# Kernel optimization log

Measured on AMD Instinct MI355X. Metric: run time of the kernel, lower is better.

## Reference

```python
import jax, jax.numpy as jnp
import numpy as np

B, S, D = 2, 1024, 2048
MLP_RATIO = 4
N_LAYERS = 2
H = D * MLP_RATIO
EPS = 1e-5


def _act_quant(x):
    # BitNet b1.58: per-token int8 absmax quantization over last dim
    scale = 127.0 / jnp.clip(jnp.max(jnp.abs(x), axis=-1, keepdims=True), EPS, None)
    return jnp.clip(jnp.round(x * scale), -128.0, 127.0) / scale


def _weight_quant(w):
    # BitNet b1.58: per-tensor ternary quantization with mean-abs scale
    scale = 1.0 / jnp.clip(jnp.mean(jnp.abs(w)), EPS, None)
    return jnp.clip(jnp.round(w * scale), -1.0, 1.0) / scale


def _ste(v, quant_fn):
    # straight-through estimator: forward quantized, backward identity
    return v + jax.lax.stop_gradient(quant_fn(v) - v)


def bit_linear(x, w, b):
    # x: [B,S,in], w: [out,in], b: [out]
    xq = _ste(x, _act_quant)
    wq = _ste(w, _weight_quant)
    return jnp.einsum('bsi,oi->bso', xq, wq) + b


def setup_inputs() -> dict:
    key = jax.random.key(0)
    ks = jax.random.split(key, 16)
    inp = {
        'x': jax.random.normal(ks[0], (B, S, D), jnp.float32),
        'y': jax.random.normal(ks[1], (B, S, D), jnp.float32),
        'z': jax.random.normal(ks[2], (B, S, D), jnp.float32),
        'focus_mask': jax.random.uniform(ks[3], (B, S, 1), jnp.float32),
        'w_in': jax.random.normal(ks[4], (D, 3 * D), jnp.float32) * 0.02,
        'b_in': jnp.zeros((D,), jnp.float32),
        'fc1_w': jax.random.normal(ks[5], (N_LAYERS, H, D), jnp.float32) * 0.02,
        'fc1_b': jnp.zeros((N_LAYERS, H), jnp.float32),
        'fc2_w': jax.random.normal(ks[6], (N_LAYERS, D, H), jnp.float32) * 0.02,
        'fc2_b': jnp.zeros((N_LAYERS, D), jnp.float32),
        'w_out': jax.random.normal(ks[7], (D, D), jnp.float32) * 0.02,
        'b_out': jnp.zeros((D,), jnp.float32),
    }
    return inp


def reference(x, y, z, focus_mask, w_in, b_in, fc1_w, fc1_b, fc2_w, fc2_b, w_out, b_out):
    h = bit_linear(jnp.concatenate([x, y, z], axis=-1), w_in, b_in)
    for l in range(N_LAYERS):
        u = jax.nn.gelu(bit_linear(h, fc1_w[l], fc1_b[l]), approximate=False)
        h = h + bit_linear(u, fc2_w[l], fc2_b[l])
    delta = bit_linear(h, w_out, b_out)
    return y + focus_mask * delta
```

## Files before the change

### kernel.cpp

```cpp
#include <hip/hip_runtime.h>

#define EPSQ 1e-5f

typedef int i32x4 __attribute__((ext_vector_type(4)));
typedef float f32x4n __attribute__((ext_vector_type(4)));

__device__ __forceinline__ unsigned short f2bf(float f) {
  unsigned int b = __builtin_bit_cast(unsigned int, f);
  b += 0x7FFFu + ((b >> 16) & 1u);
  return (unsigned short)(b >> 16);
}
__device__ __forceinline__ float bf2f(unsigned short u) {
  unsigned int b = ((unsigned int)u) << 16;
  return __builtin_bit_cast(float, b);
}
__device__ __forceinline__ int packw4(float a, float b, float c, float d, float inv) {
  int qa = (int)fminf(fmaxf(rintf(a * inv), -1.0f), 1.0f);
  int qb = (int)fminf(fmaxf(rintf(b * inv), -1.0f), 1.0f);
  int qc = (int)fminf(fmaxf(rintf(c * inv), -1.0f), 1.0f);
  int qd = (int)fminf(fmaxf(rintf(d * inv), -1.0f), 1.0f);
  return (qa & 255) | ((qb & 255) << 8) | ((qc & 255) << 16) | ((qd & 255) << 24);
}
__device__ __forceinline__ int packa4(float a, float b, float c, float d, float s) {
  int qa = (int)fminf(fmaxf(rintf(a * s), -128.0f), 127.0f);
  int qb = (int)fminf(fmaxf(rintf(b * s), -128.0f), 127.0f);
  int qc = (int)fminf(fmaxf(rintf(c * s), -128.0f), 127.0f);
  int qd = (int)fminf(fmaxf(rintf(d * s), -128.0f), 127.0f);
  return (qa & 255) | ((qb & 255) << 8) | ((qc & 255) << 16) | ((qd & 255) << 24);
}

struct WTbl {
  const float* p[6];
  unsigned char* q[6];
  unsigned int cum[7];
};

__global__ __launch_bounds__(256) void wmean_partial(WTbl tbl, double* __restrict__ part) {
  const int b = blockIdx.x;
  int t = 0;
#pragma unroll
  for (int i = 1; i < 6; ++i) t += (b >= (int)tbl.cum[i]);
  const f32x4n* __restrict__ p = (const f32x4n*)tbl.p[t];
  const unsigned int base = (unsigned)(b - (int)tbl.cum[t]) * 2048u + threadIdx.x;
  f32x4n v[8];
#pragma unroll
  for (int u = 0; u < 8; ++u) v[u] = __builtin_nontemporal_load(p + base + (unsigned)u * 256u);
  double s = 0.0;
#pragma unroll
  for (int u = 0; u < 8; ++u)
    s += (double)(fabsf(v[u][0]) + fabsf(v[u][1])) + (double)(fabsf(v[u][2]) + fabsf(v[u][3]));
  for (int off = 32; off; off >>= 1) s += __shfl_xor(s, off);
  __shared__ double wsum[4];
  if ((threadIdx.x & 63) == 0) wsum[threadIdx.x >> 6] = s;
  __syncthreads();
  if (threadIdx.x == 0) part[b] = (wsum[0] + wsum[1]) + (wsum[2] + wsum[3]);
}

__global__ __launch_bounds__(256) void wmean_final(const double* __restrict__ part,
                                                   WTbl tbl, float* wmean) {
  for (int t = 0; t < 6; ++t) {
    const int lo = (int)tbl.cum[t], hi = (int)tbl.cum[t + 1];
    double s = 0.0;
    for (int i = lo + (int)threadIdx.x; i < hi; i += 256) s += part[i];
    for (int off = 32; off; off >>= 1) s += __shfl_xor(s, off);
    __shared__ double w4[4];
    if ((threadIdx.x & 63) == 0) w4[threadIdx.x >> 6] = s;
    __syncthreads();
    if (threadIdx.x == 0) {
      const double n = (double)(hi - lo) * 8192.0;
      float m = (float)(((w4[0] + w4[1]) + (w4[2] + w4[3])) / n);
      if (m < EPSQ) m = EPSQ;
      wmean[t] = m;
    }
    __syncthreads();
  }
}

__global__ __launch_bounds__(256) void wquant(WTbl tbl, const float* wmean) {
  const int b = blockIdx.x;
  int t = 0;
#pragma unroll
  for (int i = 1; i < 6; ++i) t += (b >= (int)tbl.cum[i]);
  const float inv = 1.0f / wmean[t];
  const f32x4n* __restrict__ p = (const f32x4n*)tbl.p[t];
  int* __restrict__ q = (int*)tbl.q[t];
  const unsigned int base = (unsigned)(b - (int)tbl.cum[t]) * 2048u + threadIdx.x;
  f32x4n v[8];
#pragma unroll
  for (int u = 0; u < 8; ++u) v[u] = __builtin_nontemporal_load(p + base + (unsigned)u * 256u);
#pragma unroll
  for (int u = 0; u < 8; ++u)
    q[base + (unsigned)u * 256u] = packw4(v[u][0], v[u][1], v[u][2], v[u][3], inv);
}

__device__ __forceinline__ float block_max256(float m) {
  for (int off = 32; off; off >>= 1) m = fmaxf(m, __shfl_xor(m, off));
  __shared__ float wm[4];
  if ((threadIdx.x & 63) == 0) wm[threadIdx.x >> 6] = m;
  __syncthreads();
  return fmaxf(fmaxf(wm[0], wm[1]), fmaxf(wm[2], wm[3]));
}

__global__ __launch_bounds__(256) void aq_cat(const float* x, const float* y, const float* z,
                                              unsigned char* q, float* rsx) {
  const int row = blockIdx.x, tid = threadIdx.x;
  const float4* px = (const float4*)(x + (size_t)row * 2048);
  const float4* py = (const float4*)(y + (size_t)row * 2048);
  const float4* pz = (const float4*)(z + (size_t)row * 2048);
  float4 v[6];
  v[0] = px[tid]; v[1] = px[tid + 256];
  v[2] = py[tid]; v[3] = py[tid + 256];
  v[4] = pz[tid]; v[5] = pz[tid + 256];
  float m = 0.0f;
#pragma unroll
  for (int k = 0; k < 6; ++k)
    m = fmaxf(m, fmaxf(fmaxf(fabsf(v[k].x), fabsf(v[k].y)), fmaxf(fabsf(v[k].z), fabsf(v[k].w))));
  m = fmaxf(block_max256(m), EPSQ);
  const float s = 127.0f / m;
  if (tid == 0) rsx[row] = m / 127.0f;
  int* qr = (int*)(q + (size_t)row * 6144);
#pragma unroll
  for (int k = 0; k < 6; ++k) qr[k * 256 + tid] = packa4(v[k].x, v[k].y, v[k].z, v[k].w, s);
}

__global__ __launch_bounds__(256) void aq_bf16(const unsigned short* u, unsigned char* q, float* rsx) {
  const int row = blockIdx.x, tid = threadIdx.x;
  const uint4* pu = (const uint4*)(u + (size_t)row * 8192);
  float f[32];
#pragma unroll
  for (int k = 0; k < 4; ++k) {
    uint4 w = pu[tid + 256 * k];
    unsigned int ws4[4] = {w.x, w.y, w.z, w.w};
#pragma unroll
    for (int j = 0; j < 4; ++j) {
      f[k * 8 + j * 2 + 0] = bf2f((unsigned short)(ws4[j] & 0xFFFFu));
      f[k * 8 + j * 2 + 1] = bf2f((unsigned short)(ws4[j] >> 16));
    }
  }
  float m = 0.0f;
#pragma unroll
  for (int k = 0; k < 32; ++k) m = fmaxf(m, fabsf(f[k]));
  m = fmaxf(block_max256(m), EPSQ);
  const float s = 127.0f / m;
  if (tid == 0) rsx[row] = m / 127.0f;
  int* qp = (int*)(q + (size_t)row * 8192);
#pragma unroll
  for (int k = 0; k < 4; ++k) {
    qp[(tid + 256 * k) * 2 + 0] = packa4(f[k * 8 + 0], f[k * 8 + 1], f[k * 8 + 2], f[k * 8 + 3], s);
    qp[(tid + 256 * k) * 2 + 1] = packa4(f[k * 8 + 4], f[k * 8 + 5], f[k * 8 + 6], f[k * 8 + 7], s);
  }
}

template<int EPI>
__global__ __launch_bounds__(256) void gemm_bt(
    const unsigned char* __restrict__ A, const unsigned char* __restrict__ Bw,
    const float* rsx, const float* wmean, const float* bias,
    float* outF, unsigned short* outB, int* outI,
    int M, int N, int K, int Ksz) {
  __shared__ unsigned char As[2][128 * 128];
  __shared__ unsigned char Bs[2][128 * 128];
  const int tid = threadIdx.x;

  const int gx = gridDim.x, gy = gridDim.y;
  const int orig = blockIdx.y * gx + blockIdx.x;
  const int xcd = orig & 7;
  const int local = orig >> 3;
  const int cn = (gx >= 32) ? 8 : 4;
  const int npx = gx / cn;
  const int n = (xcd % cn) * npx + (local % npx);
  const int m = (xcd / cn) * (gy / (8 / cn)) + (local / npx);
  const int brow = m << 7;
  const int bcol = n << 7;

  const int lane = tid & 63;
  const int wv = tid >> 6;
  const int wr = (wv >> 1) << 6;
  const int wc = (wv & 1) << 6;
  const int lr = lane & 15;
  const int lg = lane >> 4;

  i32x4 acc[4][4] = {};

  const int scol = (((tid & 7) ^ ((tid >> 3) & 7)) << 4);
  const size_t koff = (size_t)blockIdx.z * Ksz;
  const unsigned char* gA0 = A + (size_t)(brow + (tid >> 3)) * K + koff + scol;
  const unsigned char* gB0 = Bw + (size_t)(bcol + (tid >> 3)) * K + koff + scol;
  const int ldst = (tid & ~63) * 16;

  auto stage = [&](int b, int kt) {
#pragma unroll
    for (int c = 0; c < 4; ++c) {
      __builtin_amdgcn_global_load_lds(
          (const __attribute__((address_space(1))) void*)(gA0 + (size_t)kt * 128 + (size_t)c * 32 * K),
          (__attribute__((address_space(3))) void*)(&As[b][c * 4096 + ldst]),
          16, 0, 0);
      __builtin_amdgcn_global_load_lds(
          (const __attribute__((address_space(1))) void*)(gB0 + (size_t)kt * 128 + (size_t)c * 32 * K),
          (__attribute__((address_space(3))) void*)(&Bs[b][c * 4096 + ldst]),
          16, 0, 0);
    }
  };

  const int nkt = Ksz >> 7;
  stage(0, 0);
  stage(1, 1);

  for (int kt = 0; kt < nkt; ++kt) {
    const int cur = kt & 1;
    if (kt + 1 < nkt) {
      asm volatile("s_waitcnt vmcnt(8)" ::: "memory");
    } else {
      asm volatile("s_waitcnt vmcnt(0)" ::: "memory");
    }
    __builtin_amdgcn_s_barrier();
    __builtin_amdgcn_sched_barrier(0);
    __builtin_amdgcn_s_setprio(1);
#pragma unroll
    for (int kk = 0; kk < 2; ++kk) {
      i32x4 af[4], bfr[4];
#pragma unroll
      for (int i = 0; i < 4; ++i) {
        const int ra = wr + i * 16 + lr;
        const int rb = wc + i * 16 + lr;
        const int ch = (((kk << 2) | lg) ^ (lr & 7)) << 4;
        af[i]  = *(const i32x4*)(&As[cur][ra * 128 + ch]);
        bfr[i] = *(const i32x4*)(&Bs[cur][rb * 128 + ch]);
      }
#pragma unroll
      for (int i = 0; i < 4; ++i)
#pragma unroll
        for (int j = 0; j < 4; ++j)
          acc[i][j] = __builtin_amdgcn_mfma_i32_16x16x64_i8(af[i], bfr[j], acc[i][j], 0, 0, 0);
    }
    __builtin_amdgcn_s_setprio(0);
    __builtin_amdgcn_sched_barrier(0);
    __builtin_amdgcn_s_barrier();
    __builtin_amdgcn_sched_barrier(0);
    if (kt + 2 < nkt) stage(cur, kt + 2);
  }

  const float mscale = (EPI == 4) ? 0.0f : wmean[0];
  int* pI = (EPI == 4) ? (outI + (size_t)blockIdx.z * M * N) : nullptr;
#pragma unroll
  for (int i = 0; i < 4; ++i) {
#pragma unroll
    for (int r = 0; r < 4; ++r) {
      const int row = brow + wr + i * 16 + lg * 4 + r;
      const float sc = (EPI == 4) ? 1.0f : rsx[row] * mscale;
#pragma unroll
      for (int j = 0; j < 4; ++j) {
        const int col = bcol + wc + j * 16 + lr;
        const size_t o = (size_t)row * N + col;
        if constexpr (EPI == 4) {
          pI[o] = acc[i][j][r];
        } else {
          float v = (float)acc[i][j][r] * sc + bias[col];
          float g = 0.5f * v * (1.0f + erff(v * 0.70710678118654752f));
          outB[o] = f2bf(g);
        }
      }
    }
  }
}

__global__ __launch_bounds__(512, 2) void gemm_fc1(
    const unsigned char* __restrict__ A,
    const unsigned char* __restrict__ Bw,
    const float* rsx, const float* wmean, const float* bias,
    unsigned short* outB, int M, int N, int K) {
  __shared__ unsigned char As[2][256 * 128];
  __shared__ unsigned char Bs[2][256 * 128];
  const int tid = threadIdx.x;

  const int gx = gridDim.x, gy = gridDim.y;
  const int orig = blockIdx.y * gx + blockIdx.x;
  const int xcd = orig & 7;
  const int local = orig >> 3;
  const int cn = (gx >= 32) ? 8 : 4;
  const int npx = gx / cn;
  const int n = (xcd % cn) * npx + (local % npx);
  const int m = (xcd / cn) * (gy / (8 / cn)) + (local / npx);
  const int brow = m << 8;
  const int bcol = n << 8;

  const int lane = tid & 63;
  const int wv = tid >> 6;
  const int wr = (wv >> 2) << 7;
  const int wc = (wv & 3) << 6;
  const int lr = lane & 15;
  const int lg = lane >> 4;

  i32x4 acc[8][4] = {};

  const int scol = (((tid & 7) ^ ((tid >> 3) & 7)) << 4);
  const unsigned char* gA0 = A + (size_t)(brow + (tid >> 3)) * K + scol;
  const unsigned char* gB0 = Bw + (size_t)(bcol + (tid >> 3)) * K + scol;
  const int ldst = (tid & ~63) * 16;

  auto stage = [&](int b, int kt) {
#pragma unroll
    for (int c = 0; c < 4; ++c) {
      __builtin_amdgcn_global_load_lds(
          (const __attribute__((address_space(1))) void*)(gA0 + (size_t)kt * 128 + (size_t)c * 64 * K),
          (__attribute__((address_space(3))) void*)(&As[b][c * 8192 + ldst]),
          16, 0, 0);
      __builtin_amdgcn_global_load_lds(
          (const __attribute__((address_space(1))) void*)(gB0 + (size_t)kt * 128 + (size_t)c * 64 * K),
          (__attribute__((address_space(3))) void*)(&Bs[b][c * 8192 + ldst]),
          16, 0, 0);
    }
  };

  const int nkt = K >> 7;
  stage(0, 0);
  stage(1, 1);

  for (int kt = 0; kt < nkt; ++kt) {
    const int cur = kt & 1;
    if (kt + 1 < nkt) {
      asm volatile("s_waitcnt vmcnt(8)" ::: "memory");
    } else {
      asm volatile("s_waitcnt vmcnt(0)" ::: "memory");
    }
    __builtin_amdgcn_s_barrier();
    __builtin_amdgcn_sched_barrier(0);
    __builtin_amdgcn_s_setprio(1);
#pragma unroll
    for (int kk = 0; kk < 2; ++kk) {
      const int ch = (((kk << 2) | lg) ^ (lr & 7)) << 4;
      i32x4 af[8], bfr[4];
#pragma unroll
      for (int i = 0; i < 8; ++i)
        af[i] = *(const i32x4*)(&As[cur][(wr + i * 16 + lr) * 128 + ch]);
#pragma unroll
      for (int j = 0; j < 4; ++j)
        bfr[j] = *(const i32x4*)(&Bs[cur][(wc + j * 16 + lr) * 128 + ch]);
#pragma unroll
      for (int i = 0; i < 8; ++i)
#pragma unroll
        for (int j = 0; j < 4; ++j)
          acc[i][j] = __builtin_amdgcn_mfma_i32_16x16x64_i8(af[i], bfr[j], acc[i][j], 0, 0, 0);
    }
    __builtin_amdgcn_s_setprio(0);
    __builtin_amdgcn_sched_barrier(0);
    __builtin_amdgcn_s_barrier();
    __builtin_amdgcn_sched_barrier(0);
    if (kt + 2 < nkt) stage(cur, kt + 2);
  }

  const float mscale = wmean[0];
#pragma unroll
  for (int i = 0; i < 8; ++i) {
#pragma unroll
    for (int r = 0; r < 4; ++r) {
      const int row = brow + wr + i * 16 + lg * 4 + r;
      const float sc = rsx[row] * mscale;
#pragma unroll
      for (int j = 0; j < 4; ++j) {
        const int col = bcol + wc + j * 16 + lr;
        float v = (float)acc[i][j][r] * sc + bias[col];
        float g = 0.5f * v * (1.0f + erff(v * 0.70710678118654752f));
        outB[(size_t)row * N + col] = f2bf(g);
      }
    }
  }
}

template<int EPI, bool WRITE_H>
__global__ __launch_bounds__(256) void reduce_qa(
    const int* __restrict__ part, int S, size_t MN,
    const float* __restrict__ wmean, const float* __restrict__ bias,
    float* __restrict__ hbuf, float* __restrict__ rsx,
    unsigned char* __restrict__ qa) {
  const int row = blockIdx.x, tid = threadIdx.x;
  const float sc = rsx[row] * wmean[0];
  const size_t rbase = (size_t)row * 2048;
  int4 v0 = *(const int4*)(part + rbase + (size_t)tid * 4);
  int4 v1 = *(const int4*)(part + rbase + (size_t)(tid + 256) * 4);
  for (int s = 1; s < S; ++s) {
    const int* ps = part + (size_t)s * MN + rbase;
    int4 a0 = *(const int4*)(ps + (size_t)tid * 4);
    int4 a1 = *(const int4*)(ps + (size_t)(tid + 256) * 4);
    v0.x += a0.x; v0.y += a0.y; v0.z += a0.z; v0.w += a0.w;
    v1.x += a1.x; v1.y += a1.y; v1.z += a1.z; v1.w += a1.w;
  }
  const float4 b0 = *(const float4*)(bias + tid * 4);
  const float4 b1 = *(const float4*)(bias + (tid + 256) * 4);
  float4 r0, r1;
  r0.x = (float)v0.x * sc + b0.x; r0.y = (float)v0.y * sc + b0.y;
  r0.z = (float)v0.z * sc + b0.z; r0.w = (float)v0.w * sc + b0.w;
  r1.x = (float)v1.x * sc + b1.x; r1.y = (float)v1.y * sc + b1.y;
  r1.z = (float)v1.z * sc + b1.z; r1.w = (float)v1.w * sc + b1.w;
  if constexpr (EPI == 2) {
    const float4 h0 = *(const float4*)(hbuf + rbase + (size_t)tid * 4);
    const float4 h1 = *(const float4*)(hbuf + rbase + (size_t)(tid + 256) * 4);
    r0.x += h0.x; r0.y += h0.y; r0.z += h0.z; r0.w += h0.w;
    r1.x += h1.x; r1.y += h1.y; r1.z += h1.z; r1.w += h1.w;
  }
  float m = fmaxf(fmaxf(fmaxf(fabsf(r0.x), fabsf(r0.y)), fmaxf(fabsf(r0.z), fabsf(r0.w))),
                  fmaxf(fmaxf(fabsf(r1.x), fabsf(r1.y)), fmaxf(fabsf(r1.z), fabsf(r1.w))));
  m = fmaxf(block_max256(m), EPSQ);
  const float s127 = 127.0f / m;
  if (tid == 0) rsx[row] = m / 127.0f;
  if constexpr (WRITE_H) {
    *(float4*)(hbuf + rbase + (size_t)tid * 4) = r0;
    *(float4*)(hbuf + rbase + (size_t)(tid + 256) * 4) = r1;
  }
  int* qp = (int*)(qa + rbase);
  qp[tid]       = packa4(r0.x, r0.y, r0.z, r0.w, s127);
  qp[tid + 256] = packa4(r1.x, r1.y, r1.z, r1.w, s127);
}

__global__ __launch_bounds__(256) void reduce_final(
    const int* __restrict__ part, int S, int N, size_t MN,
    const float* rsx, const float* wmean, const float* bias,
    const float* aux, const float* focus, float* outF) {
  const size_t i4 = ((size_t)blockIdx.x * 256 + threadIdx.x) * 4;
  if (i4 >= MN) return;
  const int row = (int)(i4 / (unsigned)N);
  const int col = (int)(i4 % (unsigned)N);
  int4 v = *(const int4*)(part + i4);
  for (int s = 1; s < S; ++s) {
    int4 p = *(const int4*)(part + (size_t)s * MN + i4);
    v.x += p.x; v.y += p.y; v.z += p.z; v.w += p.w;
  }
  const float sc = rsx[row] * wmean[0];
  const float4 b = *(const float4*)(bias + col);
  const float4 a = *(const float4*)(aux + i4);
  const float fm = focus[row];
  float4 r;
  r.x = a.x + fm * ((float)v.x * sc + b.x);
  r.y = a.y + fm * ((float)v.y * sc + b.y);
  r.z = a.z + fm * ((float)v.z * sc + b.z);
  r.w = a.w + fm * ((float)v.w * sc + b.w);
  *(float4*)(outF + i4) = r;
}

extern "C" void kernel_launch(void* const* d_in, const int* in_sizes, int n_in,
                              void* d_out, int out_size, void* d_ws, size_t ws_size,
                              hipStream_t stream) {
  const float* x     = (const float*)d_in[0];
  const float* y     = (const float*)d_in[1];
  const float* z     = (const float*)d_in[2];
  const float* fmsk  = (const float*)d_in[3];
  const float* w_in  = (const float*)d_in[4];
  const float* b_in  = (const float*)d_in[5];
  const float* fc1_w = (const float*)d_in[6];
  const float* fc1_b = (const float*)d_in[7];
  const float* fc2_w = (const float*)d_in[8];
  const float* fc2_b = (const float*)d_in[9];
  const float* w_out = (const float*)d_in[10];
  const float* b_out = (const float*)d_in[11];
  float* out = (float*)d_out;

  const int M = 2048;
  const int D = 2048, H = 8192, K3 = 6144;
  const size_t MN = (size_t)M * D;

  char* ws = (char*)d_ws;
  size_t off = 0;
  auto alloc = [&](size_t bytes) { size_t r = off; off = (off + bytes + 255) & ~(size_t)255; return r; };
  unsigned char* wq_in   = (unsigned char*)(ws + alloc((size_t)D * K3));
  unsigned char* wq_fc10 = (unsigned char*)(ws + alloc((size_t)H * D));
  unsigned char* wq_fc11 = (unsigned char*)(ws + alloc((size_t)H * D));
  unsigned char* wq_fc20 = (unsigned char*)(ws + alloc((size_t)D * H));
  unsigned char* wq_fc21 = (unsigned char*)(ws + alloc((size_t)D * H));
  unsigned char* wq_out  = (unsigned char*)(ws + alloc((size_t)D * D));
  unsigned char* qact    = (unsigned char*)(ws + alloc((size_t)M * H));
  unsigned short* ub     = (unsigned short*)(ws + alloc((size_t)M * H * 2));
  float* hbuf            = (float*)(ws + alloc(MN * 4));
  float* rsx             = (float*)(ws + alloc((size_t)M * 4));
  float* wmean           = (float*)(ws + alloc(64));
  double* part           = (double*)(ws + alloc(16384 * 8));
  int* pacc              = (int*)(ws + alloc(MN * 2 * 4));
  (void)in_sizes; (void)n_in; (void)out_size; (void)ws_size;

  WTbl tbl;
  tbl.p[0] = w_in;                  tbl.q[0] = wq_in;
  tbl.p[1] = fc1_w;                 tbl.q[1] = wq_fc10;
  tbl.p[2] = fc1_w + (size_t)H * D; tbl.q[2] = wq_fc11;
  tbl.p[3] = fc2_w;                 tbl.q[3] = wq_fc20;
  tbl.p[4] = fc2_w + (size_t)D * H; tbl.q[4] = wq_fc21;
  tbl.p[5] = w_out;                 tbl.q[5] = wq_out;
  tbl.cum[0] = 0;
  tbl.cum[1] = 1536;
  tbl.cum[2] = 1536 + 2048;
  tbl.cum[3] = 1536 + 2 * 2048;
  tbl.cum[4] = 1536 + 3 * 2048;
  tbl.cum[5] = 1536 + 4 * 2048;
  tbl.cum[6] = 1536 + 4 * 2048 + 512;

  dim3 blk(256);
  const int NCH = 10240;
  wmean_partial<<<dim3(NCH), blk, 0, stream>>>(tbl, part);
  wmean_final<<<dim3(1), blk, 0, stream>>>(part, tbl, wmean);
  wquant<<<dim3(NCH), blk, 0, stream>>>(tbl, wmean);

  aq_cat<<<dim3(M), blk, 0, stream>>>(x, y, z, qact, rsx);
  gemm_bt<4><<<dim3(D / 128, M / 128, 2), blk, 0, stream>>>(qact, wq_in, rsx, wmean + 0, b_in,
                                                            nullptr, nullptr, pacc, M, D, K3, K3 / 2);
  reduce_qa<0, true><<<dim3(M), blk, 0, stream>>>(pacc, 2, MN, wmean + 0, b_in,
                                                  hbuf, rsx, qact);

  unsigned char* wq_fc1[2] = {wq_fc10, wq_fc11};
  unsigned char* wq_fc2[2] = {wq_fc20, wq_fc21};
  for (int l = 0; l < 2; ++l) {
    gemm_fc1<<<dim3(H / 256, M / 256), dim3(512), 0, stream>>>(qact, wq_fc1[l], rsx, wmean + 1 + l,
                                                               fc1_b + (size_t)l * H, ub, M, H, D);
    aq_bf16<<<dim3(M), blk, 0, stream>>>(ub, qact, rsx);
    gemm_bt<4><<<dim3(D / 128, M / 128, 2), blk, 0, stream>>>(qact, wq_fc2[l], rsx, wmean + 3 + l,
                                                              fc2_b + (size_t)l * D,
                                                              nullptr, nullptr, pacc, M, D, H, H / 2);
    if (l == 0) {
      reduce_qa<2, true><<<dim3(M), blk, 0, stream>>>(pacc, 2, MN, wmean + 3 + l,
                                                      fc2_b + (size_t)l * D, hbuf, rsx, qact);
    } else {
      reduce_qa<2, false><<<dim3(M), blk, 0, stream>>>(pacc, 2, MN, wmean + 3 + l,
                                                       fc2_b + (size_t)l * D, hbuf, rsx, qact);
    }
  }

  gemm_bt<4><<<dim3(D / 128, M / 128, 2), blk, 0, stream>>>(qact, wq_out, rsx, wmean + 5, b_out,
                                                            nullptr, nullptr, pacc, M, D, D, D / 2);
  reduce_final<<<dim3((int)((MN / 4 + 255) / 256)), blk, 0, stream>>>(pacc, 2, D, MN, rsx, wmean + 5, b_out,
                                                                      y, fmsk, out);
}
```

Measured before the change: 437.4 us.

## Use 256x256 split-K tiles for fc2 GEMMs with nontemporal partial stores

The fc2 GEMMs move from the 128x128 two-way split-K kernel to a templated 256x256, 512-thread kernel with four-way split-K. The kernel writes int32 partial sums, and the partial buffer is enlarged to hold four slices. Partial sums are now written and read with nontemporal stores and loads, and the dead float epilogue is removed from gemm_bt. This aims at more data reuse per tile and better occupancy on the large-K fc2 GEMM, in exchange for twice the partial-sum traffic in the reduction kernel.

```diff
diff --git a/kernel.cpp b/kernel.cpp
--- a/kernel.cpp
+++ b/kernel.cpp
@@ -239,35 +239,28 @@
     if (kt + 2 < nkt) stage(cur, kt + 2);
   }
 
-  const float mscale = (EPI == 4) ? 0.0f : wmean[0];
-  int* pI = (EPI == 4) ? (outI + (size_t)blockIdx.z * M * N) : nullptr;
+  int* pI = outI + (size_t)blockIdx.z * M * N;
 #pragma unroll
   for (int i = 0; i < 4; ++i) {
 #pragma unroll
     for (int r = 0; r < 4; ++r) {
       const int row = brow + wr + i * 16 + lg * 4 + r;
-      const float sc = (EPI == 4) ? 1.0f : rsx[row] * mscale;
 #pragma unroll
       for (int j = 0; j < 4; ++j) {
         const int col = bcol + wc + j * 16 + lr;
-        const size_t o = (size_t)row * N + col;
-        if constexpr (EPI == 4) {
-          pI[o] = acc[i][j][r];
-        } else {
-          float v = (float)acc[i][j][r] * sc + bias[col];
-          float g = 0.5f * v * (1.0f + erff(v * 0.70710678118654752f));
-          outB[o] = f2bf(g);
-        }
+        __builtin_nontemporal_store(acc[i][j][r], &pI[(size_t)row * N + col]);
       }
     }
   }
-}
-
-__global__ __launch_bounds__(512, 2) void gemm_fc1(
+  (void)rsx; (void)wmean; (void)bias; (void)outF; (void)outB;
+}
+
+template<int EPI>
+__global__ __launch_bounds__(512, 2) void gemm_256(
     const unsigned char* __restrict__ A,
     const unsigned char* __restrict__ Bw,
     const float* rsx, const float* wmean, const float* bias,
-    unsigned short* outB, int M, int N, int K) {
+    unsigned short* outB, int* outI, int M, int N, int K, int Ksz) {
   __shared__ unsigned char As[2][256 * 128];
   __shared__ unsigned char Bs[2][256 * 128];
   const int tid = threadIdx.x;
@@ -293,8 +286,9 @@
   i32x4 acc[8][4] = {};
 
   const int scol = (((tid & 7) ^ ((tid >> 3) & 7)) << 4);
-  const unsigned char* gA0 = A + (size_t)(brow + (tid >> 3)) * K + scol;
-  const unsigned char* gB0 = Bw + (size_t)(bcol + (tid >> 3)) * K + scol;
+  const size_t koff = (size_t)blockIdx.z * Ksz;
+  const unsigned char* gA0 = A + (size_t)(brow + (tid >> 3)) * K + koff + scol;
+  const unsigned char* gB0 = Bw + (size_t)(bcol + (tid >> 3)) * K + koff + scol;
   const int ldst = (tid & ~63) * 16;
 
   auto stage = [&](int b, int kt) {
@@ -311,7 +305,7 @@
     }
   };
 
-  const int nkt = K >> 7;
+  const int nkt = Ksz >> 7;
   stage(0, 0);
   stage(1, 1);
 
@@ -348,19 +342,35 @@
     if (kt + 2 < nkt) stage(cur, kt + 2);
   }
 
-  const float mscale = wmean[0];
-#pragma unroll
-  for (int i = 0; i < 8; ++i) {
-#pragma unroll
-    for (int r = 0; r < 4; ++r) {
-      const int row = brow + wr + i * 16 + lg * 4 + r;
-      const float sc = rsx[row] * mscale;
-#pragma unroll
-      for (int j = 0; j < 4; ++j) {
-        const int col = bcol + wc + j * 16 + lr;
-        float v = (float)acc[i][j][r] * sc + bias[col];
-        float g = 0.5f * v * (1.0f + erff(v * 0.70710678118654752f));
-        outB[(size_t)row * N + col] = f2bf(g);
+  if constexpr (EPI == 1) {
+    const float mscale = wmean[0];
+#pragma unroll
+    for (int i = 0; i < 8; ++i) {
+#pragma unroll
+      for (int r = 0; r < 4; ++r) {
+        const int row = brow + wr + i * 16 + lg * 4 + r;
+        const float sc = rsx[row] * mscale;
+#pragma unroll
+        for (int j = 0; j < 4; ++j) {
+          const int col = bcol + wc + j * 16 + lr;
+          float v = (float)acc[i][j][r] * sc + bias[col];
+          float g = 0.5f * v * (1.0f + erff(v * 0.70710678118654752f));
+          outB[(size_t)row * N + col] = f2bf(g);
+        }
+      }
+    }
+  } else {
+    int* pI = outI + (size_t)blockIdx.z * M * N;
+#pragma unroll
+    for (int i = 0; i < 8; ++i) {
+#pragma unroll
+      for (int r = 0; r < 4; ++r) {
+        const int row = brow + wr + i * 16 + lg * 4 + r;
+#pragma unroll
+        for (int j = 0; j < 4; ++j) {
+          const int col = bcol + wc + j * 16 + lr;
+          __builtin_nontemporal_store(acc[i][j][r], &pI[(size_t)row * N + col]);
+        }
       }
     }
   }
@@ -375,22 +385,20 @@
   const int row = blockIdx.x, tid = threadIdx.x;
   const float sc = rsx[row] * wmean[0];
   const size_t rbase = (size_t)row * 2048;
-  int4 v0 = *(const int4*)(part + rbase + (size_t)tid * 4);
-  int4 v1 = *(const int4*)(part + rbase + (size_t)(tid + 256) * 4);
+  i32x4 v0 = __builtin_nontemporal_load((const i32x4*)(part + rbase) + tid);
+  i32x4 v1 = __builtin_nontemporal_load((const i32x4*)(part + rbase) + tid + 256);
   for (int s = 1; s < S; ++s) {
-    const int* ps = part + (size_t)s * MN + rbase;
-    int4 a0 = *(const int4*)(ps + (size_t)tid * 4);
-    int4 a1 = *(const int4*)(ps + (size_t)(tid + 256) * 4);
-    v0.x += a0.x; v0.y += a0.y; v0.z += a0.z; v0.w += a0.w;
-    v1.x += a1.x; v1.y += a1.y; v1.z += a1.z; v1.w += a1.w;
+    const i32x4* ps = (const i32x4*)(part + (size_t)s * MN + rbase);
+    v0 += __builtin_nontemporal_load(ps + tid);
+    v1 += __builtin_nontemporal_load(ps + tid + 256);
   }
   const float4 b0 = *(const float4*)(bias + tid * 4);
   const float4 b1 = *(const float4*)(bias + (tid + 256) * 4);
   float4 r0, r1;
-  r0.x = (float)v0.x * sc + b0.x; r0.y = (float)v0.y * sc + b0.y;
-  r0.z = (float)v0.z * sc + b0.z; r0.w = (float)v0.w * sc + b0.w;
-  r1.x = (float)v1.x * sc + b1.x; r1.y = (float)v1.y * sc + b1.y;
-  r1.z = (float)v1.z * sc + b1.z; r1.w = (float)v1.w * sc + b1.w;
+  r0.x = (float)v0[0] * sc + b0.x; r0.y = (float)v0[1] * sc + b0.y;
+  r0.z = (float)v0[2] * sc + b0.z; r0.w = (float)v0[3] * sc + b0.w;
+  r1.x = (float)v1[0] * sc + b1.x; r1.y = (float)v1[1] * sc + b1.y;
+  r1.z = (float)v1[2] * sc + b1.z; r1.w = (float)v1[3] * sc + b1.w;
   if constexpr (EPI == 2) {
     const float4 h0 = *(const float4*)(hbuf + rbase + (size_t)tid * 4);
     const float4 h1 = *(const float4*)(hbuf + rbase + (size_t)(tid + 256) * 4);
@@ -419,20 +427,18 @@
   if (i4 >= MN) return;
   const int row = (int)(i4 / (unsigned)N);
   const int col = (int)(i4 % (unsigned)N);
-  int4 v = *(const int4*)(part + i4);
-  for (int s = 1; s < S; ++s) {
-    int4 p = *(const int4*)(part + (size_t)s * MN + i4);
-    v.x += p.x; v.y += p.y; v.z += p.z; v.w += p.w;
-  }
+  i32x4 v = __builtin_nontemporal_load((const i32x4*)(part + i4));
+  for (int s = 1; s < S; ++s)
+    v += __builtin_nontemporal_load((const i32x4*)(part + (size_t)s * MN + i4));
   const float sc = rsx[row] * wmean[0];
   const float4 b = *(const float4*)(bias + col);
   const float4 a = *(const float4*)(aux + i4);
   const float fm = focus[row];
   float4 r;
-  r.x = a.x + fm * ((float)v.x * sc + b.x);
-  r.y = a.y + fm * ((float)v.y * sc + b.y);
-  r.z = a.z + fm * ((float)v.z * sc + b.z);
-  r.w = a.w + fm * ((float)v.w * sc + b.w);
+  r.x = a.x + fm * ((float)v[0] * sc + b.x);
+  r.y = a.y + fm * ((float)v[1] * sc + b.y);
+  r.z = a.z + fm * ((float)v[2] * sc + b.z);
+  r.w = a.w + fm * ((float)v[3] * sc + b.w);
   *(float4*)(outF + i4) = r;
 }
 
@@ -472,7 +478,7 @@
   float* rsx             = (float*)(ws + alloc((size_t)M * 4));
   float* wmean           = (float*)(ws + alloc(64));
   double* part           = (double*)(ws + alloc(16384 * 8));
-  int* pacc              = (int*)(ws + alloc(MN * 2 * 4));
+  int* pacc              = (int*)(ws + alloc(MN * 4 * 4));
   (void)in_sizes; (void)n_in; (void)out_size; (void)ws_size;
 
   WTbl tbl;
@@ -505,17 +511,18 @@
   unsigned char* wq_fc1[2] = {wq_fc10, wq_fc11};
   unsigned char* wq_fc2[2] = {wq_fc20, wq_fc21};
   for (int l = 0; l < 2; ++l) {
-    gemm_fc1<<<dim3(H / 256, M / 256), dim3(512), 0, stream>>>(qact, wq_fc1[l], rsx, wmean + 1 + l,
-                                                               fc1_b + (size_t)l * H, ub, M, H, D);
+    gemm_256<1><<<dim3(H / 256, M / 256), dim3(512), 0, stream>>>(qact, wq_fc1[l], rsx, wmean + 1 + l,
+                                                                  fc1_b + (size_t)l * H, ub, nullptr,
+                                                                  M, H, D, D);
     aq_bf16<<<dim3(M), blk, 0, stream>>>(ub, qact, rsx);
-    gemm_bt<4><<<dim3(D / 128, M / 128, 2), blk, 0, stream>>>(qact, wq_fc2[l], rsx, wmean + 3 + l,
-                                                              fc2_b + (size_t)l * D,
-                                                              nullptr, nullptr, pacc, M, D, H, H / 2);
+    gemm_256<4><<<dim3(D / 256, M / 256, 4), dim3(512), 0, stream>>>(qact, wq_fc2[l], rsx, wmean + 3 + l,
+                                                                     fc2_b + (size_t)l * D, nullptr, pacc,
+                                                                     M, D, H, H / 4);
     if (l == 0) {
-      reduce_qa<2, true><<<dim3(M), blk, 0, stream>>>(pacc, 2, MN, wmean + 3 + l,
+      reduce_qa<2, true><<<dim3(M), blk, 0, stream>>>(pacc, 4, MN, wmean + 3 + l,
                                                       fc2_b + (size_t)l * D, hbuf, rsx, qact);
     } else {
-      reduce_qa<2, false><<<dim3(M), blk, 0, stream>>>(pacc, 2, MN, wmean + 3 + l,
+      reduce_qa<2, false><<<dim3(M), blk, 0, stream>>>(pacc, 4, MN, wmean + 3 + l,
                                                        fc2_b + (size_t)l * D, hbuf, rsx, qact);
     }
   }
```

After: 471.9 us. +7.9%, slower.
